# Optimization experiments

Hardware: AMD Instinct MI355X
Metric: run time of the kernel (lower is better)

The kernel has to match this reference:

```python
import jax, jax.numpy as jnp
import numpy as np

TAU_CONVERGE = 0.01
N_STABLE = 2
B, L, DIM = 8, 4096, 1024
H, M = 16, 64
D_HEAD = DIM // H


def setup_inputs() -> dict:
    key = jax.random.key(0)
    k1, k2, k3, k4, k5, k6 = jax.random.split(key, 6)
    z_current = jax.random.normal(k1, (B, L, DIM), dtype=jnp.float32)
    # small perturbation so per-head velocity straddles tau_converge
    z_prev = z_current + 0.00125 * jax.random.normal(k2, (B, L, DIM), dtype=jnp.float32)
    codebook = jax.random.normal(k3, (H, M, D_HEAD), dtype=jnp.float32) * 0.02
    frozen_values = jax.random.normal(k4, (B, L, H, D_HEAD), dtype=jnp.float32)
    consecutive_converged = jax.random.randint(k5, (B, L, H), 0, 2, dtype=jnp.int32)
    crystallised = jax.random.randint(k6, (B, L, H), 0, 2) > 0
    return {
        "z_current": z_current,
        "z_prev": z_prev,
        "codebook": codebook,
        "frozen_values": frozen_values,
        "consecutive_converged": consecutive_converged,
        "crystallised": crystallised,
    }


def reference(z_current, z_prev, codebook, frozen_values, consecutive_converged, crystallised):
    """One crystallisation step: velocity -> counters -> snap-to-codebook -> enforce.

    Mirrors ConvergenceMonitor.update_and_crystallise followed by enforce(),
    with MultiHeadedCodebook.quantise(hard=True) for the codebook snap.
    All freeze/snap logic is outside the gradient graph (torch.no_grad/detach).
    """
    sg = jax.lax.stop_gradient
    zc = z_current.reshape(B, L, H, D_HEAD)   # [B,L,H,d]
    zp = z_prev.reshape(B, L, H, D_HEAD)

    # per-head velocity norm (detached in original)
    velocity = jnp.linalg.norm(sg(zc) - sg(zp), axis=-1)       # [B,L,H]
    converged = velocity < TAU_CONVERGE
    cc_new = jnp.where(converged, consecutive_converged + 1, 0)
    newly = (cc_new >= N_STABLE) & (~crystallised)             # [B,L,H] bool

    # hard nearest-neighbour quantise per head (no_grad in original)
    z_sg = sg(zc)
    cb = sg(codebook)
    # squared L2 distance: ||z||^2 - 2 z.c + ||c||^2  -> [B,L,H,M]
    d2 = (jnp.sum(z_sg * z_sg, axis=-1, keepdims=True)
          - 2.0 * jnp.einsum('blhd,hmd->blhm', z_sg, cb)
          + jnp.sum(cb * cb, axis=-1)[None, None])
    idx = jnp.argmin(d2, axis=-1)                              # [B,L,H]
    # gather nearest entries per head: codebook[h, idx[b,l,h]] -> [B,L,H,d]
    entries = cb[jnp.arange(H)[None, None, :], idx]

    # masked scatter of newly crystallised heads into frozen values
    frozen_new = jnp.where(newly[..., None], entries, sg(frozen_values))
    crystal_new = crystallised | newly

    # enforce: overwrite crystallised heads with frozen codebook values
    z_enforced = jnp.where(crystal_new[..., None], frozen_new, zc).reshape(B, L, DIM)
    return z_enforced, crystal_new, newly, cc_new, frozen_new
```

## Files before the change

kernel.cpp:

```cpp
#include <hip/hip_runtime.h>

#define BB 8
#define LL 4096
#define DIM 1024
#define HH 16
#define MM 64
#define DH 64

constexpr long long NZ = (long long)BB * LL * DIM;
constexpr long long NG = (long long)BB * LL * HH;
constexpr long long O_Z   = 0;
constexpr long long O_CRY = NZ;
constexpr long long O_NEW = NZ + NG;
constexpr long long O_CC  = NZ + 2 * NG;
constexpr long long O_FR  = NZ + 3 * NG;


#define ROWS 8

__global__ __launch_bounds__(256) void crystal_main(
    const float4* __restrict__ zc4,
    const float4* __restrict__ zp4,
    const float4* __restrict__ fr4,
    const int*    __restrict__ ccount,
    const int*    __restrict__ cryst,
    unsigned int* __restrict__ masks,
    float* __restrict__ out)
{
    __shared__ float lds_cry[ROWS * HH];
    __shared__ float lds_new[ROWS * HH];
    __shared__ float lds_cc [ROWS * HH];

    const int t   = threadIdx.x;
    const int h   = t >> 4;
    const int sub = t & 15;

    const long long row0 = (long long)blockIdx.x * ROWS;
    long long idx = row0 * (DIM / 4) + t;
    long long g   = row0 * HH + h;

    float4 zc = zc4[idx];
    float4 zp = zp4[idx];
    float4 fr = fr4[idx];
    int    cc = ccount[g];
    int    cv = cryst[g];

    unsigned int wmask = 0u;

    #pragma unroll
    for (int r = 0; r < ROWS; ++r) {
        const long long nidx = idx + (DIM / 4);
        const long long gn   = g + HH;
        float4 zcn, zpn, frn; int ccn_ = 0, cvn = 0;
        if (r < ROWS - 1) {
            zcn = zc4[nidx]; zpn = zp4[nidx]; frn = fr4[nidx];
            ccn_ = ccount[gn]; cvn = cryst[gn];
        }

        double s;
        {
            double dx = (double)zc.x - (double)zp.x;
            double dy = (double)zc.y - (double)zp.y;
            double dz = (double)zc.z - (double)zp.z;
            double dw = (double)zc.w - (double)zp.w;
            s = dx * dx + dy * dy + dz * dz + dw * dw;
        }
        s += __shfl_xor(s, 1);
        s += __shfl_xor(s, 2);
        s += __shfl_xor(s, 4);
        s += __shfl_xor(s, 8);

        const bool conv = sqrt(s) < 0.01;
        const int  ccn  = conv ? cc + 1 : 0;
        const bool cry  = cv != 0;
        const bool newly   = (ccn >= 2) && !cry;
        const bool crystal = cry || newly;

        float4 zout;
        zout.x = crystal ? fr.x : zc.x;
        zout.y = crystal ? fr.y : zc.y;
        zout.z = crystal ? fr.z : zc.z;
        zout.w = crystal ? fr.w : zc.w;

        reinterpret_cast<float4*>(out + O_Z)[idx]  = zout;
        reinterpret_cast<float4*>(out + O_FR)[idx] = fr;

        if (sub == 0) {
            lds_cry[r * HH + h] = crystal ? 1.0f : 0.0f;
            lds_new[r * HH + h] = newly   ? 1.0f : 0.0f;
            lds_cc [r * HH + h] = (float)ccn;
        }

        const unsigned long long bal = __ballot(newly && sub == 0);
        const unsigned int b4 = (unsigned int)((bal        & 1ull)       |
                                               ((bal >> 16) & 1ull) << 1 |
                                               ((bal >> 32) & 1ull) << 2 |
                                               ((bal >> 48) & 1ull) << 3);
        wmask |= b4 << (4 * r);

        zc = zcn; zp = zpn; fr = frn; cc = ccn_; cv = cvn;
        idx = nidx; g = gn;
    }

    if ((t & 63) == 0)
        masks[blockIdx.x * 4 + (t >> 6)] = wmask;

    __syncthreads();
    if (t < ROWS * HH) {
        const long long g0 = (long long)blockIdx.x * (ROWS * HH) + t;
        out[O_CRY + g0] = lds_cry[t];
        out[O_NEW + g0] = lds_new[t];
        out[O_CC  + g0] = lds_cc [t];
    }
}

#define MB_PER_CHUNK 8
#define CHUNK_ROWS  (MB_PER_CHUNK * ROWS)
#define NCHUNKS     (BB * LL / CHUNK_ROWS)
#define CBPAD 68

__global__ __launch_bounds__(64) void crystal_snap(
    const float4* __restrict__ zc4,
    const float*  __restrict__ cb,
    const unsigned int* __restrict__ masks,
    float* __restrict__ out)
{
    __shared__ float cbl[MM * CBPAD];
    __shared__ float zl[2][DH];

    const int lane = threadIdx.x;
    const int h    = blockIdx.x / NCHUNKS;
    const int c    = blockIdx.x % NCHUNKS;
    const int w    = h >> 2;
    const int h2   = h & 3;

    const int mb = c * MB_PER_CHUNK + lane;
    const unsigned int word = (lane < MB_PER_CHUNK) ? masks[mb * 4 + w] : 0u;
    unsigned int rows8 = 0u;
    #pragma unroll
    for (int r = 0; r < ROWS; ++r)
        rows8 |= ((word >> (4 * r + h2)) & 1u) << r;

    unsigned long long act = __ballot(rows8 != 0u);
    if (act == 0ull) return;

    int curl = 0; unsigned int curm8 = 0u;
    auto next_bl = [&]() -> long long {
        while (curm8 == 0u) {
            if (act == 0ull) return -1;
            curl = __ffsll(act) - 1; act &= act - 1;
            curm8 = __shfl(rows8, curl);
        }
        const int r = __ffs(curm8) - 1; curm8 &= curm8 - 1;
        return (long long)(c * MB_PER_CHUNK + curl) * ROWS + r;
    };

    long long bl0 = next_bl();
    long long seg0 = bl0 * (DIM / 4) + h * (DH / 4);
    float4 zv0;
    if (lane < 16) zv0 = zc4[seg0 + lane];

    const float4* cbh4 = reinterpret_cast<const float4*>(cb + (long long)h * MM * DH);
    #pragma unroll
    for (int i = 0; i < 16; ++i) {
        const int gidx = i * 64 + lane;
        const float4 v = cbh4[gidx];
        const int m  = gidx >> 4;
        const int k4 = (gidx & 15) * 4;
        float* dst = &cbl[m * CBPAD + k4];
        dst[0] = v.x; dst[1] = v.y; dst[2] = v.z; dst[3] = v.w;
    }

    long long bl1 = next_bl();
    long long seg1 = bl1 * (DIM / 4) + h * (DH / 4);
    float4 zv1;
    if (bl1 >= 0 && lane < 16) zv1 = zc4[seg1 + lane];

    float4 crw[16];
    #pragma unroll
    for (int k = 0; k < 16; ++k)
        crw[k] = *reinterpret_cast<const float4*>(&cbl[lane * CBPAD + k * 4]);

    int p = 0;

    while (bl0 >= 0) {
        if (lane < 16) reinterpret_cast<float4*>(zl[p])[lane] = zv0;

        const long long bl2 = next_bl();
        const long long seg2 = bl2 * (DIM / 4) + h * (DH / 4);
        float4 zv2;
        if (bl2 >= 0 && lane < 16) zv2 = zc4[seg2 + lane];

        float f0 = 0.f, f1 = 0.f, f2 = 0.f, f3 = 0.f;
        #pragma unroll
        for (int k = 0; k < 16; ++k) {
            const float4 zk = reinterpret_cast<const float4*>(zl[p])[k];
            const float q0 = zk.x - crw[k].x;
            const float q1 = zk.y - crw[k].y;
            const float q2 = zk.z - crw[k].z;
            const float q3 = zk.w - crw[k].w;
            f0 += q0 * q0; f1 += q1 * q1; f2 += q2 * q2; f3 += q3 * q3;
        }
        float b1 = (f0 + f1) + (f2 + f3);
        int   i1 = lane;
        float b2 = 3.4e38f;
        #pragma unroll
        for (int m2 = 1; m2 <= 32; m2 <<= 1) {
            const float ob1 = __shfl_xor(b1, m2);
            const int   oi1 = __shfl_xor(i1, m2);
            const float ob2 = __shfl_xor(b2, m2);
            const bool take = (ob1 < b1) || (ob1 == b1 && oi1 < i1);
            const float loser = take ? b1 : ob1;
            if (take) { b1 = ob1; i1 = oi1; }
            b2 = fminf(fminf(b2, ob2), loser);
        }
        int bidx = i1;

        if (b2 - b1 <= 1e-3f) {
            const float* crow = &cbl[lane * CBPAD];
            const float* zrow = zl[p];
            double a0 = 0.0, a1 = 0.0, a2 = 0.0, a3 = 0.0;
            #pragma unroll
            for (int d = 0; d < DH; d += 4) {
                double q0 = (double)zrow[d + 0] - (double)crow[d + 0];
                double q1 = (double)zrow[d + 1] - (double)crow[d + 1];
                double q2 = (double)zrow[d + 2] - (double)crow[d + 2];
                double q3 = (double)zrow[d + 3] - (double)crow[d + 3];
                a0 += q0 * q0; a1 += q1 * q1; a2 += q2 * q2; a3 += q3 * q3;
            }
            double best = (a0 + a1) + (a2 + a3);
            int bx = lane;
            #pragma unroll
            for (int m2 = 1; m2 <= 32; m2 <<= 1) {
                double ob = __shfl_xor(best, m2);
                int    oi = __shfl_xor(bx, m2);
                if (ob < best || (ob == best && oi < bx)) { best = ob; bx = oi; }
            }
            bidx = bx;
        }

        if (lane < 16) {
            const float* er = &cbl[bidx * CBPAD + lane * 4];
            float4 ev;
            ev.x = er[0]; ev.y = er[1]; ev.z = er[2]; ev.w = er[3];
            reinterpret_cast<float4*>(out + O_Z)[seg0 + lane]  = ev;
            reinterpret_cast<float4*>(out + O_FR)[seg0 + lane] = ev;
        }

        bl0 = bl1; seg0 = seg1; zv0 = zv1;
        bl1 = bl2; seg1 = seg2; zv1 = zv2;
        p ^= 1;
    }
}

extern "C" void kernel_launch(void* const* d_in, const int* in_sizes, int n_in,
                              void* d_out, int out_size, void* d_ws, size_t ws_size,
                              hipStream_t stream) {
    const float4* zc4 = (const float4*)d_in[0];
    const float4* zp4 = (const float4*)d_in[1];
    const float*  cb  = (const float*)d_in[2];
    const float4* fr4 = (const float4*)d_in[3];
    const int*    cc  = (const int*)d_in[4];
    const int*    cry = (const int*)d_in[5];
    float* out = (float*)d_out;
    unsigned int* masks = (unsigned int*)d_ws;

    hipLaunchKernelGGL(crystal_main, dim3((BB * LL) / ROWS), dim3(256), 0, stream,
                       zc4, zp4, fr4, cc, cry, masks, out);
    hipLaunchKernelGGL(crystal_snap, dim3(HH * NCHUNKS), dim3(64), 0, stream,
                       zc4, cb, masks, out);
}
```

Baseline: 198.9 us.

## Split velocity and enforce passes into separate kernels via crystal bitmasks

Splits the fused main kernel into a velocity/counter kernel that emits both newly and crystal bitmasks, plus a separate enforce kernel that rereads z_current and frozen_values to write z and frozen outputs. The intent is to shrink per-kernel register and memory pressure so each pass streams more efficiently. In exchange z_current is read twice from global memory, with an extra kernel launch and another mask array in the workspace.

```diff
diff --git a/kernel.cpp b/kernel.cpp
--- a/kernel.cpp
+++ b/kernel.cpp
@@ -18,13 +18,13 @@
 
 #define ROWS 8
 
-__global__ __launch_bounds__(256) void crystal_main(
+__global__ __launch_bounds__(256) void crystal_vel(
     const float4* __restrict__ zc4,
     const float4* __restrict__ zp4,
-    const float4* __restrict__ fr4,
     const int*    __restrict__ ccount,
     const int*    __restrict__ cryst,
-    unsigned int* __restrict__ masks,
+    unsigned int* __restrict__ masks_new,
+    unsigned int* __restrict__ masks_cry,
     float* __restrict__ out)
 {
     __shared__ float lds_cry[ROWS * HH];
@@ -41,19 +41,19 @@
 
     float4 zc = zc4[idx];
     float4 zp = zp4[idx];
-    float4 fr = fr4[idx];
     int    cc = ccount[g];
     int    cv = cryst[g];
 
-    unsigned int wmask = 0u;
+    unsigned int wmask_n = 0u;
+    unsigned int wmask_c = 0u;
 
     #pragma unroll
     for (int r = 0; r < ROWS; ++r) {
         const long long nidx = idx + (DIM / 4);
         const long long gn   = g + HH;
-        float4 zcn, zpn, frn; int ccn_ = 0, cvn = 0;
+        float4 zcn, zpn; int ccn_ = 0, cvn = 0;
         if (r < ROWS - 1) {
-            zcn = zc4[nidx]; zpn = zp4[nidx]; frn = fr4[nidx];
+            zcn = zc4[nidx]; zpn = zp4[nidx];
             ccn_ = ccount[gn]; cvn = cryst[gn];
         }
 
@@ -76,34 +76,34 @@
         const bool newly   = (ccn >= 2) && !cry;
         const bool crystal = cry || newly;
 
-        float4 zout;
-        zout.x = crystal ? fr.x : zc.x;
-        zout.y = crystal ? fr.y : zc.y;
-        zout.z = crystal ? fr.z : zc.z;
-        zout.w = crystal ? fr.w : zc.w;
-
-        reinterpret_cast<float4*>(out + O_Z)[idx]  = zout;
-        reinterpret_cast<float4*>(out + O_FR)[idx] = fr;
-
         if (sub == 0) {
             lds_cry[r * HH + h] = crystal ? 1.0f : 0.0f;
             lds_new[r * HH + h] = newly   ? 1.0f : 0.0f;
             lds_cc [r * HH + h] = (float)ccn;
         }
 
-        const unsigned long long bal = __ballot(newly && sub == 0);
-        const unsigned int b4 = (unsigned int)((bal        & 1ull)       |
-                                               ((bal >> 16) & 1ull) << 1 |
-                                               ((bal >> 32) & 1ull) << 2 |
-                                               ((bal >> 48) & 1ull) << 3);
-        wmask |= b4 << (4 * r);
-
-        zc = zcn; zp = zpn; fr = frn; cc = ccn_; cv = cvn;
+        const unsigned long long baln = __ballot(newly && sub == 0);
+        const unsigned int bn = (unsigned int)((baln        & 1ull)       |
+                                               ((baln >> 16) & 1ull) << 1 |
+                                               ((baln >> 32) & 1ull) << 2 |
+                                               ((baln >> 48) & 1ull) << 3);
+        wmask_n |= bn << (4 * r);
+
+        const unsigned long long balc = __ballot(crystal && sub == 0);
+        const unsigned int bc = (unsigned int)((balc        & 1ull)       |
+                                               ((balc >> 16) & 1ull) << 1 |
+                                               ((balc >> 32) & 1ull) << 2 |
+                                               ((balc >> 48) & 1ull) << 3);
+        wmask_c |= bc << (4 * r);
+
+        zc = zcn; zp = zpn; cc = ccn_; cv = cvn;
         idx = nidx; g = gn;
     }
 
-    if ((t & 63) == 0)
-        masks[blockIdx.x * 4 + (t >> 6)] = wmask;
+    if ((t & 63) == 0) {
+        masks_new[blockIdx.x * 4 + (t >> 6)] = wmask_n;
+        masks_cry[blockIdx.x * 4 + (t >> 6)] = wmask_c;
+    }
 
     __syncthreads();
     if (t < ROWS * HH) {
@@ -111,6 +111,45 @@
         out[O_CRY + g0] = lds_cry[t];
         out[O_NEW + g0] = lds_new[t];
         out[O_CC  + g0] = lds_cc [t];
+    }
+}
+
+__global__ __launch_bounds__(256) void crystal_enf(
+    const float4* __restrict__ zc4,
+    const float4* __restrict__ fr4,
+    const unsigned int* __restrict__ masks_cry,
+    float* __restrict__ out)
+{
+    const int t  = threadIdx.x;
+    const int h2 = (t >> 4) & 3;
+    const int wv = t >> 6;
+
+    const unsigned int cw = masks_cry[blockIdx.x * 4 + wv];
+
+    const long long row0 = (long long)blockIdx.x * ROWS;
+    long long idx = row0 * (DIM / 4) + t;
+
+    float4 zc = zc4[idx];
+    float4 fr = fr4[idx];
+
+    #pragma unroll
+    for (int r = 0; r < ROWS; ++r) {
+        const long long nidx = idx + (DIM / 4);
+        float4 zcn, frn;
+        if (r < ROWS - 1) { zcn = zc4[nidx]; frn = fr4[nidx]; }
+
+        const bool crystal = (cw >> (4 * r + h2)) & 1u;
+
+        float4 zout;
+        zout.x = crystal ? fr.x : zc.x;
+        zout.y = crystal ? fr.y : zc.y;
+        zout.z = crystal ? fr.z : zc.z;
+        zout.w = crystal ? fr.w : zc.w;
+
+        reinterpret_cast<float4*>(out + O_Z)[idx]  = zout;
+        reinterpret_cast<float4*>(out + O_FR)[idx] = fr;
+
+        zc = zcn; fr = frn; idx = nidx;
     }
 }
 
@@ -263,10 +302,13 @@
     const int*    cc  = (const int*)d_in[4];
     const int*    cry = (const int*)d_in[5];
     float* out = (float*)d_out;
-    unsigned int* masks = (unsigned int*)d_ws;
-
-    hipLaunchKernelGGL(crystal_main, dim3((BB * LL) / ROWS), dim3(256), 0, stream,
-                       zc4, zp4, fr4, cc, cry, masks, out);
+    unsigned int* masks_new = (unsigned int*)d_ws;
+    unsigned int* masks_cry = (unsigned int*)d_ws + 16384;
+
+    hipLaunchKernelGGL(crystal_vel, dim3((BB * LL) / ROWS), dim3(256), 0, stream,
+                       zc4, zp4, cc, cry, masks_new, masks_cry, out);
+    hipLaunchKernelGGL(crystal_enf, dim3((BB * LL) / ROWS), dim3(256), 0, stream,
+                       zc4, fr4, masks_cry, out);
     hipLaunchKernelGGL(crystal_snap, dim3(HH * NCHUNKS), dim3(64), 0, stream,
-                       zc4, cb, masks, out);
+                       zc4, cb, masks_new, out);
 }
```

After: 226.1 us. +13.7%, slower.
